# Kernel optimization log

Measured on AMD Instinct MI355X. Metric: run time of the kernel, lower is better.

Reference implementation:

```python
import jax, jax.numpy as jnp
import numpy as np

B, C_IN, C_OUT, K, H, W = 16, 256, 512, 7, 64, 64
PAD = K // 2


def setup_inputs() -> dict:
    key = jax.random.key(0)
    k1, k2, k3 = jax.random.split(key, 3)
    x = jax.random.normal(k1, (B, C_IN, H, W), dtype=jnp.float32)
    # depthwise weight: [out_channels=C_IN, in_channels//groups=1, k, k]
    fan_dw = 1 * K * K
    dw_w = jax.random.normal(k2, (C_IN, 1, K, K), dtype=jnp.float32) * np.sqrt(2.0 / fan_dw)
    dw_b = jnp.zeros((C_IN,), dtype=jnp.float32)
    # pointwise weight: [C_OUT, C_IN, 1, 1]
    pw_w = jax.random.normal(k3, (C_OUT, C_IN, 1, 1), dtype=jnp.float32) * np.sqrt(2.0 / C_IN)
    pw_b = jnp.zeros((C_OUT,), dtype=jnp.float32)
    return {"x": x, "dw_w": dw_w, "dw_b": dw_b, "pw_w": pw_w, "pw_b": pw_b}


def reference(x, dw_w, dw_b, pw_w, pw_b):
    # Depthwise conv (groups == C_in): cross-correlation, same as the torch
    # unfold+einsum construction with zero padding k//2.
    y = jax.lax.conv_general_dilated(
        x, dw_w,
        window_strides=(1, 1),
        padding=[(PAD, PAD), (PAD, PAD)],
        feature_group_count=C_IN,
        dimension_numbers=("NCHW", "OIHW", "NCHW"),
    )
    y = y + dw_b[None, :, None, None]
    # Pointwise 1x1 conv == per-pixel GEMM over channels.
    out = jnp.einsum("bchw,oc->bohw", y, pw_w[:, :, 0, 0])
    out = out + pw_b[None, :, None, None]
    return out
```

## Files before the change

### kernel.cpp

```cpp
#include <hip/hip_runtime.h>

typedef unsigned short US;
typedef __bf16 bf16x8 __attribute__((ext_vector_type(8)));
typedef float f32x4 __attribute__((ext_vector_type(4)));

__device__ __forceinline__ US f2bf(float f) {
  union { float f; unsigned u; } v; v.f = f;
  unsigned r = v.u + 0x7fffu + ((v.u >> 16) & 1u);
  return (US)(r >> 16);
}
__device__ __forceinline__ float blo(unsigned u) {
  union { unsigned u; float f; } v; v.u = u << 16; return v.f;
}
__device__ __forceinline__ float bhi(unsigned u) {
  union { unsigned u; float f; } v; v.u = u & 0xffff0000u; return v.f;
}

__global__ __launch_bounds__(256) void k_convw(const float* __restrict__ pw,
                                               US* __restrict__ wb) {
  int i = (blockIdx.x * 256 + threadIdx.x) * 4;
  float4 v = *(const float4*)(pw + i);
  ushort4 s;
  s.x = f2bf(v.x); s.y = f2bf(v.y); s.z = f2bf(v.z); s.w = f2bf(v.w);
  *(ushort4*)(wb + i) = s;
}

__global__ __launch_bounds__(512, 4) void k_dw(const float* __restrict__ x,
                                               const float* __restrict__ dww,
                                               const float* __restrict__ dwb,
                                               US* __restrict__ y8) {
  const int bid = blockIdx.x;
  const int rg  = bid & 3;
  const int cg  = (bid >> 2) & 31;
  const int b   = bid >> 7;
  const int t   = threadIdx.x;
  const int w   = t >> 6;
  const int l   = t & 63;
  const int g   = l >> 4;
  const int cb  = l & 15;
  const int c   = __builtin_amdgcn_readfirstlane(cg * 8 + w);
  const float* xp = x + ((size_t)b * 256 + c) * 4096;

  __shared__ US xl[8][24][64];
  __shared__ US t8[8][1024];

  const int r0 = rg * 16;

  {
    const int rowl0 = l >> 3;
    const int colb  = (l & 7) * 8;
#pragma unroll
    for (int it = 0; it < 3; ++it) {
      const int rowl = it * 8 + rowl0;
      const int gr   = r0 - 3 + rowl;
      const int grc  = min(max(gr, 0), 63);
      const float* gp = xp + grc * 64 + colb;
      float4 f0 = *(const float4*)(gp);
      float4 f1 = *(const float4*)(gp + 4);
      uint4 pk;
      pk.x = ((unsigned)f2bf(f0.y) << 16) | f2bf(f0.x);
      pk.y = ((unsigned)f2bf(f0.w) << 16) | f2bf(f0.z);
      pk.z = ((unsigned)f2bf(f1.y) << 16) | f2bf(f1.x);
      pk.w = ((unsigned)f2bf(f1.w) << 16) | f2bf(f1.z);
      *(uint4*)&xl[w][rowl][colb] = pk;
    }
  }

  float wv[49];
  const float* wp = dww + c * 49;
#pragma unroll
  for (int i = 0; i < 49; ++i) wv[i] = wp[i];
  const float bias = dwb[c];

  asm volatile("s_waitcnt vmcnt(0) lgkmcnt(0)" ::: "memory");
  __builtin_amdgcn_wave_barrier();

  const int bcx  = cb * 4;
  const bool colL = (bcx >= 4);
  const bool colR = (bcx < 60);
  const int offL  = colL ? -4 : 0;
  const int offR  = colR ?  4 : 0;

  float acc[4][4];
#pragma unroll
  for (int o = 0; o < 4; ++o)
#pragma unroll
    for (int q = 0; q < 4; ++q) acc[o][q] = bias;

#pragma unroll
  for (int j = 0; j < 10; ++j) {
    const int gr = r0 + g * 4 - 3 + j;
    const bool rowOK = ((unsigned)gr < 64u);
    const US* rp = &xl[w][g * 4 + j][bcx];
    uint2 va = *(const uint2*)(rp + offL);
    uint2 vb = *(const uint2*)(rp);
    uint2 vc = *(const uint2*)(rp + offR);
    const bool okL = rowOK && colL;
    const bool okR = rowOK && colR;
    va.x = okL   ? va.x : 0u;  va.y = okL   ? va.y : 0u;
    vb.x = rowOK ? vb.x : 0u;  vb.y = rowOK ? vb.y : 0u;
    vc.x = okR   ? vc.x : 0u;  vc.y = okR   ? vc.y : 0u;
    float L[12];
    L[0] = blo(va.x); L[1]  = bhi(va.x); L[2]  = blo(va.y); L[3]  = bhi(va.y);
    L[4] = blo(vb.x); L[5]  = bhi(vb.x); L[6]  = blo(vb.y); L[7]  = bhi(vb.y);
    L[8] = blo(vc.x); L[9]  = bhi(vc.x); L[10] = blo(vc.y); L[11] = bhi(vc.y);
#pragma unroll
    for (int o = 0; o < 4; ++o) {
      if (j - o >= 0 && j - o <= 6) {
        const int kh = j - o;
#pragma unroll
        for (int kw = 0; kw < 7; ++kw) {
          const float wk = wv[kh * 7 + kw];
#pragma unroll
          for (int q = 0; q < 4; ++q)
            acc[o][q] = fmaf(L[q + kw + 1], wk, acc[o][q]);
        }
      }
    }
  }

#pragma unroll
  for (int o = 0; o < 4; ++o) {
    ushort4 s;
    s.x = f2bf(acc[o][0]); s.y = f2bf(acc[o][1]);
    s.z = f2bf(acc[o][2]); s.w = f2bf(acc[o][3]);
    *(ushort4*)&t8[w][(g * 4 + o) * 64 + bcx] = s;
  }
  __syncthreads();

  unsigned rc8[8];
#pragma unroll
  for (int c2 = 0; c2 < 8; ++c2) rc8[c2] = *(const unsigned*)&t8[c2][2 * t];
  uint4 A, B2;
  A.x  = __builtin_amdgcn_perm(rc8[1], rc8[0], 0x05040100u);
  A.y  = __builtin_amdgcn_perm(rc8[3], rc8[2], 0x05040100u);
  A.z  = __builtin_amdgcn_perm(rc8[5], rc8[4], 0x05040100u);
  A.w  = __builtin_amdgcn_perm(rc8[7], rc8[6], 0x05040100u);
  B2.x = __builtin_amdgcn_perm(rc8[1], rc8[0], 0x07060302u);
  B2.y = __builtin_amdgcn_perm(rc8[3], rc8[2], 0x07060302u);
  B2.z = __builtin_amdgcn_perm(rc8[5], rc8[4], 0x07060302u);
  B2.w = __builtin_amdgcn_perm(rc8[7], rc8[6], 0x07060302u);
  US* yb = y8 + (((size_t)b * 32 + cg) * 4096 + r0 * 64) * 8 + (size_t)t * 16;
  *(uint4*)(yb)     = A;
  *(uint4*)(yb + 8) = B2;
}

__global__ __launch_bounds__(256, 2) void k_pw(const US* __restrict__ y8,
                                               const US* __restrict__ wb,
                                               const float* __restrict__ pwb,
                                               float* __restrict__ out) {
  const int bid = blockIdx.x;
  const int s   = ((bid & 7) << 8) | (bid >> 3);
  const int b   = s >> 7;
  const int rr  = s & 127;
  const int nt  = rr >> 2;
  const int mt  = rr & 3;
  const int o0  = mt * 128;
  const int hw0 = nt * 128;

  __shared__ US lsA[2][128][72];
  __shared__ US lsB[2][128][72];
  const int tid  = threadIdx.x;
  const int lane = tid & 63;
  const int wid  = tid >> 6;
  const int wm   = wid >> 1, wn = wid & 1;
  const int strow = tid >> 3;
  const int scg   = tid & 7;
  const int bg    = tid >> 5;
  const int bl    = tid & 31;

  const f32x4 fzero = {0.f, 0.f, 0.f, 0.f};
  f32x4 acc[4][4];
#pragma unroll
  for (int m = 0; m < 4; ++m)
#pragma unroll
    for (int n = 0; n < 4; ++n) acc[m][n] = fzero;

  uint4 ra[4], rb[4];
#pragma unroll
  for (int i = 0; i < 4; ++i) {
    ra[i] = *(const uint4*)(wb + (size_t)(o0 + i * 32 + strow) * 256 + scg * 8);
    rb[i] = *(const uint4*)(y8 + ((size_t)(b * 32 + bg) * 4096 + hw0 + bl + 32 * i) * 8);
  }
#pragma unroll
  for (int i = 0; i < 4; ++i) {
    *(uint4*)&lsA[0][i * 32 + strow][scg * 8] = ra[i];
    *(uint4*)&lsB[0][bl + 32 * i][bg * 8]     = rb[i];
  }
  __syncthreads();

  for (int kt = 0; kt < 4; ++kt) {
    const int cur = kt & 1;
    if (kt < 3) {
      const int ck = (kt + 1) * 64;
#pragma unroll
      for (int i = 0; i < 4; ++i) {
        ra[i] = *(const uint4*)(wb + (size_t)(o0 + i * 32 + strow) * 256 + ck + scg * 8);
        rb[i] = *(const uint4*)(y8 + ((size_t)(b * 32 + (ck >> 3) + bg) * 4096 + hw0 + bl + 32 * i) * 8);
      }
    }
    bf16x8 af[2][4], bfr[2][4];
#pragma unroll
    for (int kk = 0; kk < 2; ++kk) {
      const int kcol = kk * 32 + (lane >> 4) * 8;
#pragma unroll
      for (int m = 0; m < 4; ++m)
        af[kk][m] = *reinterpret_cast<const bf16x8*>(&lsA[cur][wm * 64 + m * 16 + (lane & 15)][kcol]);
#pragma unroll
      for (int n = 0; n < 4; ++n)
        bfr[kk][n] = *reinterpret_cast<const bf16x8*>(&lsB[cur][wn * 64 + n * 16 + (lane & 15)][kcol]);
    }
#pragma unroll
    for (int kk = 0; kk < 2; ++kk)
#pragma unroll
      for (int m = 0; m < 4; ++m)
#pragma unroll
        for (int n = 0; n < 4; ++n)
          acc[m][n] = __builtin_amdgcn_mfma_f32_16x16x32_bf16(bfr[kk][n], af[kk][m], acc[m][n], 0, 0, 0);

    if (kt < 3) {
#pragma unroll
      for (int i = 0; i < 4; ++i) {
        *(uint4*)&lsA[cur ^ 1][i * 32 + strow][scg * 8] = ra[i];
        *(uint4*)&lsB[cur ^ 1][bl + 32 * i][bg * 8]     = rb[i];
      }
      __syncthreads();
    }
  }

#pragma unroll
  for (int m = 0; m < 4; ++m) {
    const int o  = o0 + wm * 64 + m * 16 + (lane & 15);
    const float bv = pwb[o];
    float* orow = out + (((size_t)b * 512 + o) * 4096) + hw0 + wn * 64 + (lane >> 4) * 4;
#pragma unroll
    for (int n = 0; n < 4; ++n) {
      f32x4 v = acc[m][n];
      v[0] += bv; v[1] += bv; v[2] += bv; v[3] += bv;
      *(f32x4*)(orow + n * 16) = v;
    }
  }
}

extern "C" void kernel_launch(void* const* d_in, const int* in_sizes, int n_in,
                              void* d_out, int out_size, void* d_ws, size_t ws_size,
                              hipStream_t stream) {
  const float* x   = (const float*)d_in[0];
  const float* dww = (const float*)d_in[1];
  const float* dwb = (const float*)d_in[2];
  const float* pww = (const float*)d_in[3];
  const float* pwb = (const float*)d_in[4];
  float* out = (float*)d_out;

  char* ws = (char*)d_ws;
  US* y8  = (US*)ws;
  US* wbf = (US*)(ws + 33554432);

  k_convw<<<128,  256, 0, stream>>>(pww, wbf);
  k_dw   <<<2048, 512, 0, stream>>>(x, dww, dwb, y8);
  k_pw   <<<2048, 256, 0, stream>>>(y8, wbf, pwb, out);
}
```

Measured before the change: 72.72 us.

## Keep full-K activation tile resident in LDS and loop over output-channel tiles

The pointwise GEMM kernel now loads a whole 128-pixel by 256-channel activation tile into LDS once per block, then iterates over four 128-row weight tiles, each with the full K=256 reduction. Blocks grow to 1024 threads and the grid shrinks to 512 blocks. This is meant to stop reloading the same activation slice from global memory four times across separate blocks. In exchange it drops the double-buffered prefetch, so each weight-tile load is exposed behind a barrier, and LDS use per block grows to about 135KB, which limits occupancy.

```diff
diff --git a/kernel.cpp b/kernel.cpp
--- a/kernel.cpp
+++ b/kernel.cpp
@@ -145,100 +145,84 @@
   *(uint4*)(yb + 8) = B2;
 }
 
-__global__ __launch_bounds__(256, 2) void k_pw(const US* __restrict__ y8,
-                                               const US* __restrict__ wb,
-                                               const float* __restrict__ pwb,
-                                               float* __restrict__ out) {
+__global__ __launch_bounds__(1024, 4) void k_pw(const US* __restrict__ y8,
+                                                const US* __restrict__ wb,
+                                                const float* __restrict__ pwb,
+                                                float* __restrict__ out) {
   const int bid = blockIdx.x;
-  const int s   = ((bid & 7) << 8) | (bid >> 3);
-  const int b   = s >> 7;
-  const int rr  = s & 127;
-  const int nt  = rr >> 2;
-  const int mt  = rr & 3;
-  const int o0  = mt * 128;
+  const int s   = ((bid & 7) << 6) | (bid >> 3);
+  const int b   = s >> 5;
+  const int nt  = s & 31;
   const int hw0 = nt * 128;
 
-  __shared__ US lsA[2][128][72];
-  __shared__ US lsB[2][128][72];
-  const int tid  = threadIdx.x;
-  const int lane = tid & 63;
-  const int wid  = tid >> 6;
-  const int wm   = wid >> 1, wn = wid & 1;
-  const int strow = tid >> 3;
-  const int scg   = tid & 7;
-  const int bg    = tid >> 5;
-  const int bl    = tid & 31;
+  __shared__ US sB[128][264];
+  __shared__ US sA[128][264];
+
+  const int t    = threadIdx.x;
+  const int lane = t & 63;
+  const int wid  = t >> 6;
+  const int wm   = wid >> 2;
+  const int wn   = wid & 3;
+
+#pragma unroll
+  for (int it = 0; it < 4; ++it) {
+    const int idx = it * 1024 + t;
+    const int cg  = idx >> 7;
+    const int px  = idx & 127;
+    uint4 v = *(const uint4*)(y8 + ((size_t)(b * 32 + cg) * 4096 + hw0 + px) * 8);
+    *(uint4*)&sB[px][cg * 8] = v;
+  }
 
   const f32x4 fzero = {0.f, 0.f, 0.f, 0.f};
-  f32x4 acc[4][4];
-#pragma unroll
-  for (int m = 0; m < 4; ++m)
-#pragma unroll
-    for (int n = 0; n < 4; ++n) acc[m][n] = fzero;
-
-  uint4 ra[4], rb[4];
-#pragma unroll
-  for (int i = 0; i < 4; ++i) {
-    ra[i] = *(const uint4*)(wb + (size_t)(o0 + i * 32 + strow) * 256 + scg * 8);
-    rb[i] = *(const uint4*)(y8 + ((size_t)(b * 32 + bg) * 4096 + hw0 + bl + 32 * i) * 8);
-  }
-#pragma unroll
-  for (int i = 0; i < 4; ++i) {
-    *(uint4*)&lsA[0][i * 32 + strow][scg * 8] = ra[i];
-    *(uint4*)&lsB[0][bl + 32 * i][bg * 8]     = rb[i];
-  }
-  __syncthreads();
-
-  for (int kt = 0; kt < 4; ++kt) {
-    const int cur = kt & 1;
-    if (kt < 3) {
-      const int ck = (kt + 1) * 64;
-#pragma unroll
-      for (int i = 0; i < 4; ++i) {
-        ra[i] = *(const uint4*)(wb + (size_t)(o0 + i * 32 + strow) * 256 + ck + scg * 8);
-        rb[i] = *(const uint4*)(y8 + ((size_t)(b * 32 + (ck >> 3) + bg) * 4096 + hw0 + bl + 32 * i) * 8);
+
+  for (int mt = 0; mt < 4; ++mt) {
+    const int o0 = mt * 128;
+#pragma unroll
+    for (int it = 0; it < 4; ++it) {
+      const int idx = it * 1024 + t;
+      const int o   = idx >> 5;
+      const int ch  = idx & 31;
+      uint4 v = *(const uint4*)(wb + (size_t)(o0 + o) * 256 + ch * 8);
+      *(uint4*)&sA[o][ch * 8] = v;
+    }
+    __syncthreads();
+
+    f32x4 acc[2][2];
+#pragma unroll
+    for (int m = 0; m < 2; ++m)
+#pragma unroll
+      for (int n = 0; n < 2; ++n) acc[m][n] = fzero;
+
+#pragma unroll
+    for (int kk = 0; kk < 8; ++kk) {
+      const int kcol = kk * 32 + (lane >> 4) * 8;
+      bf16x8 af[2], bfr[2];
+#pragma unroll
+      for (int m = 0; m < 2; ++m)
+        af[m] = *reinterpret_cast<const bf16x8*>(&sA[wm * 32 + m * 16 + (lane & 15)][kcol]);
+#pragma unroll
+      for (int n = 0; n < 2; ++n)
+        bfr[n] = *reinterpret_cast<const bf16x8*>(&sB[wn * 32 + n * 16 + (lane & 15)][kcol]);
+#pragma unroll
+      for (int m = 0; m < 2; ++m)
+#pragma unroll
+        for (int n = 0; n < 2; ++n)
+          acc[m][n] = __builtin_amdgcn_mfma_f32_16x16x32_bf16(bfr[n], af[m], acc[m][n], 0, 0, 0);
+    }
+
+#pragma unroll
+    for (int m = 0; m < 2; ++m) {
+      const int o  = o0 + wm * 32 + m * 16 + (lane & 15);
+      const float bv = pwb[o];
+      float* orow = out + (((size_t)b * 512 + o) * 4096) + hw0 + wn * 32 + (lane >> 4) * 4;
+#pragma unroll
+      for (int n = 0; n < 2; ++n) {
+        f32x4 v = acc[m][n];
+        v[0] += bv; v[1] += bv; v[2] += bv; v[3] += bv;
+        *(f32x4*)(orow + n * 16) = v;
       }
     }
-    bf16x8 af[2][4], bfr[2][4];
-#pragma unroll
-    for (int kk = 0; kk < 2; ++kk) {
-      const int kcol = kk * 32 + (lane >> 4) * 8;
-#pragma unroll
-      for (int m = 0; m < 4; ++m)
-        af[kk][m] = *reinterpret_cast<const bf16x8*>(&lsA[cur][wm * 64 + m * 16 + (lane & 15)][kcol]);
-#pragma unroll
-      for (int n = 0; n < 4; ++n)
-        bfr[kk][n] = *reinterpret_cast<const bf16x8*>(&lsB[cur][wn * 64 + n * 16 + (lane & 15)][kcol]);
-    }
-#pragma unroll
-    for (int kk = 0; kk < 2; ++kk)
-#pragma unroll
-      for (int m = 0; m < 4; ++m)
-#pragma unroll
-        for (int n = 0; n < 4; ++n)
-          acc[m][n] = __builtin_amdgcn_mfma_f32_16x16x32_bf16(bfr[kk][n], af[kk][m], acc[m][n], 0, 0, 0);
-
-    if (kt < 3) {
-#pragma unroll
-      for (int i = 0; i < 4; ++i) {
-        *(uint4*)&lsA[cur ^ 1][i * 32 + strow][scg * 8] = ra[i];
-        *(uint4*)&lsB[cur ^ 1][bl + 32 * i][bg * 8]     = rb[i];
-      }
-      __syncthreads();
-    }
-  }
-
-#pragma unroll
-  for (int m = 0; m < 4; ++m) {
-    const int o  = o0 + wm * 64 + m * 16 + (lane & 15);
-    const float bv = pwb[o];
-    float* orow = out + (((size_t)b * 512 + o) * 4096) + hw0 + wn * 64 + (lane >> 4) * 4;
-#pragma unroll
-    for (int n = 0; n < 4; ++n) {
-      f32x4 v = acc[m][n];
-      v[0] += bv; v[1] += bv; v[2] += bv; v[3] += bv;
-      *(f32x4*)(orow + n * 16) = v;
-    }
+    __syncthreads();
   }
 }
 
@@ -258,5 +242,5 @@
 
   k_convw<<<128,  256, 0, stream>>>(pww, wbf);
   k_dw   <<<2048, 512, 0, stream>>>(x, dww, dwb, y8);
-  k_pw   <<<2048, 256, 0, stream>>>(y8, wbf, pwb, out);
-}
+  k_pw   <<<512, 1024, 0, stream>>>(y8, wbf, pwb, out);
+}
```

Measured after the change: 76.90 us. +5.7%, slower.
